# Kernel tuning notes

Measured on AMD Instinct MI355X. Metric: run time of the kernel, lower is better.

The kernel has to match this reference:

```python
import jax, jax.numpy as jnp
import numpy as np
from jax import lax

NPOINT = 1024
K = 32
GN_GROUPS = 32
EPS = 1e-5


def farthest_point_sample(xyz, npoint):
    # xyz: (B,N,3) -> idx (B,npoint). Deterministic start at index 0.
    B, N, _ = xyz.shape
    dist0 = jnp.full((B, N), 1e10, dtype=xyz.dtype)
    far0 = jnp.zeros((B,), dtype=jnp.int32)
    barange = jnp.arange(B)

    def step(carry, _):
        dist, far = carry
        centroid = xyz[barange, far][:, None, :]              # (B,1,3)
        d = jnp.sum((xyz - centroid) ** 2, axis=-1)           # (B,N)
        dist = jnp.minimum(dist, d)
        far_new = jnp.argmax(dist, axis=-1).astype(jnp.int32)
        return (dist, far_new), far

    _, idxs = lax.scan(step, (dist0, far0), None, length=npoint)
    return idxs.T  # (B,npoint)


def conv1x1(x, w, b):
    # x: (B,Cin,M,K), w: (Cout,Cin)
    return jnp.einsum('oc,bcmk->bomk', w, x) + b[None, :, None, None]


def group_norm(x, gamma, beta, groups):
    B, C, M, Kk = x.shape
    xg = x.reshape(B, groups, C // groups, M, Kk)
    mu = xg.mean(axis=(2, 3, 4), keepdims=True)
    var = xg.var(axis=(2, 3, 4), keepdims=True)
    xg = (xg - mu) * lax.rsqrt(var + EPS)
    x = xg.reshape(B, C, M, Kk)
    return x * gamma[None, :, None, None] + beta[None, :, None, None]


def setup_inputs() -> dict:
    key = jax.random.key(0)
    ks = jax.random.split(key, 4)
    B, N, Cin = 16, 8192, 64
    hid, out_ch, in_total = 64, 128, 3 + Cin
    return {
        'xyz': jax.random.normal(ks[0], (B, N, 3), jnp.float32),
        'feat': jax.random.normal(ks[1], (B, N, Cin), jnp.float32),
        'w1': jax.random.normal(ks[2], (hid, in_total), jnp.float32) * 0.1,
        'b1': jnp.zeros((hid,), jnp.float32),
        'g1w': jnp.ones((hid,), jnp.float32),
        'g1b': jnp.zeros((hid,), jnp.float32),
        'w2': jax.random.normal(ks[3], (out_ch, hid), jnp.float32) * 0.1,
        'b2': jnp.zeros((out_ch,), jnp.float32),
        'g2w': jnp.ones((out_ch,), jnp.float32),
        'g2b': jnp.zeros((out_ch,), jnp.float32),
    }


def reference(xyz, feat, w1, b1, g1w, g1b, w2, b2, g2w, g2b):
    B, N, _ = xyz.shape
    M = min(NPOINT, N)
    k = min(K, N)

    fps_idx = farthest_point_sample(lax.stop_gradient(xyz), M)   # (B,M) ints
    batch = jnp.arange(B)[:, None]
    centroids = xyz[batch, fps_idx]                              # (B,M,3)

    # kNN via squared distances (same ordering as cdist p=2)
    d2 = (jnp.sum(centroids ** 2, -1)[:, :, None]
          + jnp.sum(xyz ** 2, -1)[:, None, :]
          - 2.0 * jnp.einsum('bmd,bnd->bmn', centroids, xyz))    # (B,M,N)
    knn_idx = lax.top_k(-d2, k)[1]                               # (B,M,k)

    b3 = jnp.arange(B)[:, None, None]
    group_xyz = xyz[b3, knn_idx]                                 # (B,M,k,3)
    delta = group_xyz - centroids[:, :, None, :]
    gfeat = feat[b3, knn_idx]                                    # (B,M,k,Cin)
    gf = jnp.concatenate([delta, gfeat], axis=-1)                # (B,M,k,3+Cin)
    x = jnp.transpose(gf, (0, 3, 1, 2))                          # (B,C,M,k)

    x = jax.nn.relu(group_norm(conv1x1(x, w1, b1), g1w, g1b, GN_GROUPS))
    x = jax.nn.relu(group_norm(conv1x1(x, w2, b2), g2w, g2b, GN_GROUPS))
    out = jnp.max(x, axis=-1)                                    # (B,out_ch,M)
    new_feat = jnp.transpose(out, (0, 2, 1))                     # (B,M,out_ch)
    return (centroids, new_feat)
```

## Files before the change

kernel.cpp:

```cpp
#include <hip/hip_runtime.h>
#include <cstdint>

#define BB 16
#define NN 8192
#define MM 1024
#define KNN 32
#define CIN 64
#define HID 64
#define OCH 128

#define KNN_OFF   0u
#define SUM1_OFF  524288u
#define SUM2_OFF  526336u
#define A1_OFF    530432u
#define D1_OFF    531456u
#define A2_OFF    532480u
#define D2_OFF    534528u
#define W2B_OFF   536576u
#define W1B_OFF   540672u
#define Y1_OFF    543744u
#define PTS4_OFF  Y1_OFF
#define FEAT16_OFF (Y1_OFF + 16777216u)

typedef unsigned long long u64;
typedef float f32x4 __attribute__((ext_vector_type(4)));
typedef float f32x2 __attribute__((ext_vector_type(2)));
typedef short bf16x8 __attribute__((ext_vector_type(8)));

__device__ __forceinline__ unsigned short f2bf(float f) {
  union { float f; unsigned u; } v; v.f = f;
  unsigned r = v.u + 0x7FFFu + ((v.u >> 16) & 1u);
  return (unsigned short)(r >> 16);
}

__device__ __forceinline__ float bf2f(unsigned short u) {
  return __uint_as_float((unsigned)u << 16);
}

__global__ __launch_bounds__(256) void k0_init(const float* __restrict__ xyz,
                                               const float* __restrict__ feat,
                                               const float* __restrict__ w1,
                                               const float* __restrict__ w2,
                                               float* __restrict__ ws) {
  int t = blockIdx.x * 256 + threadIdx.x;
  if (t < 12288) ws[SUM1_OFF + t] = 0.0f;
  if (t < 4096) {
    unsigned lo = f2bf(w2[2 * t]);
    unsigned hi = f2bf(w2[2 * t + 1]);
    ((unsigned*)(ws + W2B_OFF))[t] = lo | (hi << 16);
  }
  if (t < 6144) {
    int n = t / 96, kk = t % 96;
    float val = 0.0f;
    if (kk < 3) val = w1[n * 67 + kk];
    else if (kk >= 4 && kk < 68) val = w1[n * 67 + kk - 1];
    ((unsigned short*)(ws + W1B_OFF))[t] = f2bf(val);
  }
  if (t < BB * NN) {
    #pragma clang fp contract(off)
    float x = xyz[(size_t)t * 3], y = xyz[(size_t)t * 3 + 1], z = xyz[(size_t)t * 3 + 2];
    ((float4*)(ws + PTS4_OFF))[t] = make_float4(x, y, z, (x * x + y * y) + z * z);
  }
  if (t < 4194304) {
    float2 fv = *(const float2*)(feat + 2 * (size_t)t);
    unsigned lo = f2bf(fv.x), hi = f2bf(fv.y);
    ((unsigned*)(ws + FEAT16_OFF))[t] = lo | (hi << 16);
  }
}

__device__ __forceinline__ u64 wave_max_u64(u64 v) {
  #define DPP_RND(ctrl, rm)                                                     \
  {                                                                             \
    int lo_ = __builtin_amdgcn_update_dpp(0, (int)(unsigned)(v & 0xFFFFFFFFull),\
                                          ctrl, rm, 0xf, true);                 \
    int hi_ = __builtin_amdgcn_update_dpp(0, (int)(unsigned)(v >> 32),          \
                                          ctrl, rm, 0xf, true);                 \
    u64 o_ = ((u64)(unsigned)hi_ << 32) | (unsigned)lo_;                        \
    v = o_ > v ? o_ : v;                                                        \
  }
  DPP_RND(0x111, 0xf)
  DPP_RND(0x112, 0xf)
  DPP_RND(0x114, 0xf)
  DPP_RND(0x118, 0xf)
  DPP_RND(0x142, 0xa)
  DPP_RND(0x143, 0xc)
  #undef DPP_RND
  return v;
}

__global__ __launch_bounds__(256) void fps_kernel(const float* __restrict__ xyz,
                                                  float* __restrict__ cent) {
  #pragma clang fp contract(off)
  __shared__ float4 sp4[NN];
  __shared__ u64 slots[MM];
  __shared__ u64 wred[2][4];
  const int b = blockIdx.x, tid = threadIdx.x;
  const int w = tid >> 6;
  const float* xp = xyz + (size_t)b * NN * 3;
  f32x2 px[16], py[16], pz[16];
  float dist0[16], dist1[16];
  #pragma unroll
  for (int i = 0; i < 16; ++i) {
    int n0 = tid + (2 * i) * 256, n1 = tid + (2 * i + 1) * 256;
    float x0 = xp[n0 * 3], y0 = xp[n0 * 3 + 1], z0 = xp[n0 * 3 + 2];
    float x1 = xp[n1 * 3], y1 = xp[n1 * 3 + 1], z1 = xp[n1 * 3 + 2];
    px[i] = (f32x2){x0, x1}; py[i] = (f32x2){y0, y1}; pz[i] = (f32x2){z0, z1};
    sp4[n0] = make_float4(x0, y0, z0, 0.0f);
    sp4[n1] = make_float4(x1, y1, z1, 0.0f);
    dist0[i] = 1e10f; dist1[i] = 1e10f;
  }
  __syncthreads();
  int far = 0;
  for (int step = 0; step < MM; ++step) {
    float4 c4 = sp4[far];
    f32x2 cx = (f32x2){c4.x, c4.x}, cy = (f32x2){c4.y, c4.y}, cz = (f32x2){c4.z, c4.z};
    float best = -1.0f;
    #pragma unroll
    for (int i = 0; i < 16; ++i) {
      f32x2 dx = px[i] - cx, dy = py[i] - cy, dz = pz[i] - cz;
      f32x2 d = (dx * dx + dy * dy) + dz * dz;
      float dm0 = fminf(dist0[i], d.x);
      float dm1 = fminf(dist1[i], d.y);
      dist0[i] = dm0; dist1[i] = dm1;
      best = fmaxf(fmaxf(best, dm0), dm1);
    }
    unsigned sel[16];
    #pragma unroll
    for (int i = 0; i < 16; ++i) {
      unsigned s0 = (dist0[i] == best) ? (unsigned)(2 * i) : 63u;
      unsigned s1 = (dist1[i] == best) ? (unsigned)(2 * i + 1) : 63u;
      sel[i] = s0 < s1 ? s0 : s1;
    }
    #pragma unroll
    for (int st = 8; st >= 1; st >>= 1)
      #pragma unroll
      for (int i = 0; i < st; ++i)
        sel[i] = sel[i] < sel[i + st] ? sel[i] : sel[i + st];
    int bi = tid + (int)(sel[0] << 8);
    u64 key = ((u64)__float_as_uint(best) << 32) | (unsigned)(8191 - bi);
    key = wave_max_u64(key);
    const int p = step & 1;
    if ((tid & 63) == 63) wred[p][w] = key;
    __syncthreads();
    u64 k0 = wred[p][0], k1 = wred[p][1], k2 = wred[p][2], k3 = wred[p][3];
    u64 m01 = k0 > k1 ? k0 : k1;
    u64 m23 = k2 > k3 ? k2 : k3;
    u64 bk = m01 > m23 ? m01 : m23;
    if (tid == 0) slots[step] = bk;
    far = 8191 - (int)(unsigned)(bk & 0xFFFFFFFFull);
  }
  __syncthreads();
  float* co = cent + (size_t)b * MM * 3;
  for (int s = tid; s < MM; s += 256) {
    int fs = (s == 0) ? 0 : (8191 - (int)(unsigned)(slots[s - 1] & 0xFFFFFFFFull));
    float4 c = sp4[fs];
    co[s * 3 + 0] = c.x; co[s * 3 + 1] = c.y; co[s * 3 + 2] = c.z;
  }
}

__global__ __launch_bounds__(512) void knn_kernel(const float4* __restrict__ pts4,
                                                  const float* __restrict__ cent,
                                                  int* __restrict__ knnout) {
  #pragma clang fp contract(off)
  __shared__ __align__(16) char smem[65536];
  unsigned* blo = (unsigned*)smem;
  unsigned* bhi = (unsigned*)(smem + 32768);
  u64* marea = (u64*)smem;
  const int tid = threadIdx.x;
  const int lane = tid & 63;
  const int w = tid >> 6;
  const int b = blockIdx.x >> 4;
  const int m = ((blockIdx.x & 15) << 6) + lane;
  const float* cp = cent + ((size_t)b * MM + m) * 3;
  float cx = cp[0], cy = cp[1], cz = cp[2];
  float cn2 = (cx * cx + cy * cy) + cz * cz;
  u64 key[32];
  {
    u64 initk = ((u64)(__float_as_uint(3e38f) ^ 0x80000000u) << 32) | 0xFFFFFFFFull;
    #pragma unroll
    for (int j = 0; j < 32; ++j) key[j] = initk;
  }
  float kthf = 3e38f;

  auto insert = [&](u64 cand) {
    bool cprev = false; u64 kprev = 0;
    #pragma unroll
    for (int j = 0; j < 32; ++j) {
      bool cj = cand < key[j];
      u64 cur = key[j];
      u64 nv = cj ? cand : cur;
      key[j] = cprev ? kprev : nv;
      cprev = cj; kprev = cur;
    }
    unsigned hb = (unsigned)(key[31] >> 32);
    unsigned ob = (hb & 0x80000000u) ? (hb ^ 0x80000000u) : ~hb;
    kthf = __uint_as_float(ob);
  };

  int cnt = 0;
  auto flush = [&]() {
    int mc = cnt;
    #pragma unroll
    for (int off = 1; off < 64; off <<= 1) { int o = __shfl_xor(mc, off); mc = o > mc ? o : mc; }
    for (int i = 0; i < mc; ++i) {
      u64 cand = ((u64)bhi[i * 512 + tid] << 32) | blo[i * 512 + tid];
      if (i < cnt && cand < key[31]) insert(cand);
    }
    cnt = 0;
  };

  const int nbase = __builtin_amdgcn_readfirstlane(w * 1024);
  const float4* pb = pts4 + (size_t)b * NN + nbase;
  for (int n0 = 0; n0 < 1024; n0 += 8) {
    #pragma unroll
    for (int j = 0; j < 8; ++j) {
      int n = n0 + j;
      float4 p = pb[n];
      float dot = fmaf(cz, p.z, fmaf(cy, p.y, cx * p.x));
      float d2 = (cn2 + p.w) - 2.0f * dot;
      if (d2 <= kthf) {
        unsigned db = __float_as_uint(d2);
        unsigned fk = db ^ (((int)db < 0) ? 0xFFFFFFFFu : 0x80000000u);
        blo[cnt * 512 + tid] = (unsigned)(nbase + n);
        bhi[cnt * 512 + tid] = fk;
        cnt++;
      }
    }
    if (__ballot(cnt >= 9)) flush();
  }
  flush();
  __syncthreads();

  auto publish = [&](int a) {
    u64* ap = marea + a * 2048;
    #pragma unroll
    for (int j = 0; j < 32; ++j) ap[j * 64 + lane] = key[j];
  };
  auto merge_from = [&](int a) {
    u64* ap = marea + a * 2048;
    for (int j = 0; j < 32; ++j) {
      u64 cand = ap[j * 64 + lane];
      if (cand < key[31]) insert(cand);
    }
  };
  if (w & 1) publish(w >> 1);
  __syncthreads();
  if (!(w & 1)) merge_from(w >> 1);
  __syncthreads();
  if (w == 2) publish(0);
  if (w == 6) publish(1);
  __syncthreads();
  if (w == 0) merge_from(0);
  if (w == 4) merge_from(1);
  __syncthreads();
  if (w == 4) publish(0);
  __syncthreads();
  if (w == 0) {
    merge_from(0);
    int* op = knnout + ((size_t)b * MM + m) * KNN;
    #pragma unroll
    for (int j = 0; j < 32; ++j) op[j] = (int)(key[j] & 0xFFFFFFFFull);
  }
}

__global__ __launch_bounds__(256) void conv1_kernel(const float* __restrict__ xyz,
                                                    const unsigned short* __restrict__ feat16,
                                                    const float* __restrict__ cent,
                                                    const int* __restrict__ knn,
                                                    const unsigned short* __restrict__ w1b,
                                                    const float* __restrict__ b1,
                                                    float* __restrict__ y1,
                                                    float* __restrict__ sums1) {
  __shared__ __align__(16) unsigned short gsm[4][32 * 104];
  __shared__ float s1acc[64], q1acc[64];
  const int tid = threadIdx.x, lane = tid & 63, w = tid >> 6;
  const int wid = blockIdx.x * 4 + w;
  const int b = wid >> 10;
  unsigned short* gf = gsm[w];

  if (tid < 64) { s1acc[tid] = 0.0f; q1acc[tid] = 0.0f; }
  __syncthreads();

  int idxv = 0;
  if (lane < 32) idxv = knn[(size_t)wid * 32 + lane];

  {
    int row = lane >> 1, h = (lane & 1) * 16;
    ushort4 z4 = {0, 0, 0, 0};
    *(ushort4*)(gf + row * 104 + 64 + h + 0)  = z4;
    *(ushort4*)(gf + row * 104 + 64 + h + 4)  = z4;
    *(ushort4*)(gf + row * 104 + 64 + h + 8)  = z4;
    *(ushort4*)(gf + row * 104 + 64 + h + 12) = z4;
  }
  const float* cp = cent + (size_t)wid * 3;
  float ccx = cp[0], ccy = cp[1], ccz = cp[2];
  if (lane < 32) {
    const float* pp = xyz + ((size_t)b * NN + idxv) * 3;
    ushort4 dv;
    dv.x = f2bf(pp[0] - ccx); dv.y = f2bf(pp[1] - ccy); dv.z = f2bf(pp[2] - ccz);
    dv.w = 0;
    *(ushort4*)(gf + lane * 104) = dv;
  }
  const unsigned short* fb = feat16 + (size_t)b * NN * 64;
  #pragma unroll
  for (int i = 0; i < 4; ++i) {
    int v = i * 64 + lane;
    int row = v >> 3, part = v & 7;
    int ridx = __shfl(idxv, row);
    uint4 fv = *(const uint4*)(fb + (size_t)ridx * 64 + part * 8);
    *(uint2*)(gf + row * 104 + 4 + part * 8)     = make_uint2(fv.x, fv.y);
    *(uint2*)(gf + row * 104 + 4 + part * 8 + 4) = make_uint2(fv.z, fv.w);
  }
  __builtin_amdgcn_s_waitcnt(0);
  __builtin_amdgcn_wave_barrier();

  const int quad = lane >> 4, lr = lane & 15;
  bf16x8 bw[4][3];
  float b1v[4];
  #pragma unroll
  for (int nt = 0; nt < 4; ++nt) {
    #pragma unroll
    for (int ks = 0; ks < 3; ++ks)
      bw[nt][ks] = *(const bf16x8*)(w1b + (size_t)(nt * 16 + lr) * 96 + ks * 32 + quad * 8);
    b1v[nt] = b1[nt * 16 + lr];
  }
  f32x4 acc[2][4];
  #pragma unroll
  for (int mt = 0; mt < 2; ++mt)
    #pragma unroll
    for (int nt = 0; nt < 4; ++nt)
      acc[mt][nt] = (f32x4){0.f, 0.f, 0.f, 0.f};
  #pragma unroll
  for (int ks = 0; ks < 3; ++ks) {
    bf16x8 a0 = *(const bf16x8*)(gf + (0 + lr) * 104 + ks * 32 + quad * 8);
    bf16x8 a1 = *(const bf16x8*)(gf + (16 + lr) * 104 + ks * 32 + quad * 8);
    #pragma unroll
    for (int nt = 0; nt < 4; ++nt) {
      acc[0][nt] = __builtin_amdgcn_mfma_f32_16x16x32_bf16(a0, bw[nt][ks], acc[0][nt], 0, 0, 0);
      acc[1][nt] = __builtin_amdgcn_mfma_f32_16x16x32_bf16(a1, bw[nt][ks], acc[1][nt], 0, 0, 0);
    }
  }
  unsigned short* yo16 = (unsigned short*)(y1 + (size_t)wid * 1024);
  float s_nt[4] = {0.f, 0.f, 0.f, 0.f};
  float q_nt[4] = {0.f, 0.f, 0.f, 0.f};
  #pragma unroll
  for (int mt = 0; mt < 2; ++mt)
    #pragma unroll
    for (int rg = 0; rg < 4; ++rg) {
      int row = mt * 16 + quad * 4 + rg;
      #pragma unroll
      for (int nt = 0; nt < 4; ++nt) {
        float z = acc[mt][nt][rg] + b1v[nt];
        yo16[row * 64 + nt * 16 + lr] = f2bf(z);
        s_nt[nt] += z;
        q_nt[nt] = fmaf(z, z, q_nt[nt]);
      }
    }
  #pragma unroll
  for (int nt = 0; nt < 4; ++nt) {
    float s = s_nt[nt], q = q_nt[nt];
    s += __shfl_xor(s, 16); s += __shfl_xor(s, 32);
    q += __shfl_xor(q, 16); q += __shfl_xor(q, 32);
    if (quad == 0) {
      atomicAdd(&s1acc[nt * 16 + lr], s);
      atomicAdd(&q1acc[nt * 16 + lr], q);
    }
  }
  __syncthreads();
  if (tid < 64) {
    atomicAdd(&sums1[b * 128 + tid], s1acc[tid]);
    atomicAdd(&sums1[b * 128 + 64 + tid], q1acc[tid]);
  }
}

struct Conv2Frag {
  bf16x8 bfr[8][2];
  float  b2v[8];
};

__device__ __forceinline__ void load_w2_frags(const unsigned short* __restrict__ w2b,
                                              const float* __restrict__ b2,
                                              int lane, Conv2Frag& F) {
  const int quad = lane >> 4, lr = lane & 15;
  #pragma unroll
  for (int nt = 0; nt < 8; ++nt) {
    #pragma unroll
    for (int t = 0; t < 2; ++t)
      F.bfr[nt][t] = *(const bf16x8*)(w2b + (size_t)(nt * 16 + lr) * 64 + t * 32 + quad * 8);
    F.b2v[nt] = b2[nt * 16 + lr];
  }
}

__device__ __forceinline__ void conv2_wave_mfma(const float* __restrict__ y1,
                                                const float* a1s,
                                                const float* d1s,
                                                unsigned short* __restrict__ hrow,
                                                int wid, int lane,
                                                const Conv2Frag& F,
                                                f32x4 acc[2][8]) {
  const int quad = lane >> 4, lr = lane & 15;
  const int r = lane >> 1, c0 = (lane & 1) * 32;
  const unsigned short* yrow16 =
      (const unsigned short*)(y1 + (size_t)wid * 1024) + r * 64 + c0;
  const float4* ap = (const float4*)(a1s + c0);
  const float4* dp = (const float4*)(d1s + c0);
  #pragma unroll
  for (int gg = 0; gg < 4; ++gg) {
    bf16x8 yv = *(const bf16x8*)(yrow16 + gg * 8);
    float4 av0 = ap[gg * 2],     dv0 = dp[gg * 2];
    float4 av1 = ap[gg * 2 + 1], dv1 = dp[gg * 2 + 1];
    ushort4 s0, s1;
    s0.x = f2bf(fmaxf(0.0f, fmaf(bf2f((unsigned short)yv[0]), av0.x, dv0.x)));
    s0.y = f2bf(fmaxf(0.0f, fmaf(bf2f((unsigned short)yv[1]), av0.y, dv0.y)));
    s0.z = f2bf(fmaxf(0.0f, fmaf(bf2f((unsigned short)yv[2]), av0.z, dv0.z)));
    s0.w = f2bf(fmaxf(0.0f, fmaf(bf2f((unsigned short)yv[3]), av0.w, dv0.w)));
    s1.x = f2bf(fmaxf(0.0f, fmaf(bf2f((unsigned short)yv[4]), av1.x, dv1.x)));
    s1.y = f2bf(fmaxf(0.0f, fmaf(bf2f((unsigned short)yv[5]), av1.y, dv1.y)));
    s1.z = f2bf(fmaxf(0.0f, fmaf(bf2f((unsigned short)yv[6]), av1.z, dv1.z)));
    s1.w = f2bf(fmaxf(0.0f, fmaf(bf2f((unsigned short)yv[7]), av1.w, dv1.w)));
    *(ushort4*)(hrow + r * 72 + c0 + 8 * gg)     = s0;
    *(ushort4*)(hrow + r * 72 + c0 + 8 * gg + 4) = s1;
  }
  __builtin_amdgcn_s_waitcnt(0);
  __builtin_amdgcn_wave_barrier();
  #pragma unroll
  for (int mt = 0; mt < 2; ++mt)
    #pragma unroll
    for (int nt = 0; nt < 8; ++nt)
      acc[mt][nt] = (f32x4){0.f, 0.f, 0.f, 0.f};
  #pragma unroll
  for (int t = 0; t < 2; ++t) {
    bf16x8 a0 = *(const bf16x8*)(hrow + (0 + lr) * 72 + t * 32 + quad * 8);
    bf16x8 a1f = *(const bf16x8*)(hrow + (16 + lr) * 72 + t * 32 + quad * 8);
    #pragma unroll
    for (int nt = 0; nt < 8; ++nt) {
      acc[0][nt] = __builtin_amdgcn_mfma_f32_16x16x32_bf16(a0,  F.bfr[nt][t], acc[0][nt], 0, 0, 0);
      acc[1][nt] = __builtin_amdgcn_mfma_f32_16x16x32_bf16(a1f, F.bfr[nt][t], acc[1][nt], 0, 0, 0);
    }
  }
}

__global__ __launch_bounds__(256) void conv2_stats_kernel(float* __restrict__ y1,
                                                          const float* __restrict__ sums1,
                                                          const float* __restrict__ g1w,
                                                          const float* __restrict__ g1b,
                                                          const unsigned short* __restrict__ w2b,
                                                          const float* __restrict__ b2,
                                                          float* __restrict__ sums2) {
  __shared__ __align__(16) unsigned short hsm[4][32 * 72];
  __shared__ float sacc[128], qacc[128];
  __shared__ float a1s[64], d1s[64];
  const int tid = threadIdx.x, lane = tid & 63, w = tid >> 6;
  const int wid = blockIdx.x * 4 + w;
  const int b = blockIdx.x >> 8;
  if (tid < 128) { sacc[tid] = 0.0f; qacc[tid] = 0.0f; }
  if (tid < 64) {
    int c = tid, g = c >> 1;
    float S = sums1[b * 128 + g * 2] + sums1[b * 128 + g * 2 + 1];
    float Q = sums1[b * 128 + 64 + g * 2] + sums1[b * 128 + 64 + g * 2 + 1];
    float mu = S * (1.0f / 65536.0f);
    float var = Q * (1.0f / 65536.0f) - mu * mu;
    float rs = 1.0f / sqrtf(var + 1e-5f);
    float ga = g1w[c];
    a1s[c] = rs * ga;
    d1s[c] = g1b[c] - mu * rs * ga;
  }
  __syncthreads();
  Conv2Frag F;
  load_w2_frags(w2b, b2, lane, F);
  f32x4 acc[2][8];
  conv2_wave_mfma(y1, a1s, d1s, hsm[w], wid, lane, F, acc);
  const int lr = lane & 15;
  float zmx[8], zmn[8];
  #pragma unroll
  for (int nt = 0; nt < 8; ++nt) {
    float s = 0, q = 0, mx = -3e38f, mn = 3e38f;
    #pragma unroll
    for (int mt = 0; mt < 2; ++mt)
      #pragma unroll
      for (int rg = 0; rg < 4; ++rg) {
        float z = acc[mt][nt][rg] + F.b2v[nt];
        s += z; q = fmaf(z, z, q);
        mx = fmaxf(mx, z); mn = fminf(mn, z);
      }
    atomicAdd(&sacc[nt * 16 + lr], s);
    atomicAdd(&qacc[nt * 16 + lr], q);
    mx = fmaxf(mx, __shfl_xor(mx, 16)); mx = fmaxf(mx, __shfl_xor(mx, 32));
    mn = fminf(mn, __shfl_xor(mn, 16)); mn = fminf(mn, __shfl_xor(mn, 32));
    zmx[nt] = mx; zmn[nt] = mn;
  }
  if (lane < 16) {
    float* zp = y1 + (size_t)wid * 1024;
    #pragma unroll
    for (int nt = 0; nt < 8; ++nt) {
      zp[nt * 16 + lr] = zmx[nt];
      zp[128 + nt * 16 + lr] = zmn[nt];
    }
  }
  __syncthreads();
  if (tid < 128) {
    atomicAdd(&sums2[b * 256 + tid], sacc[tid]);
    atomicAdd(&sums2[b * 256 + 128 + tid], qacc[tid]);
  }
}

__global__ __launch_bounds__(256) void final_lite(const float* __restrict__ y1,
                                                  const float* __restrict__ sums2,
                                                  const float* __restrict__ g2w,
                                                  const float* __restrict__ g2b,
                                                  float* __restrict__ nf) {
  __shared__ float a2s[128], d2s[128];
  const int tid = threadIdx.x;
  const int wid0 = blockIdx.x * 2;
  const int b = wid0 >> 10;
  if (tid < 128) {
    int c = tid, g = c >> 2;
    float S = ((sums2[b * 256 + g * 4] + sums2[b * 256 + g * 4 + 1])
               + sums2[b * 256 + g * 4 + 2]) + sums2[b * 256 + g * 4 + 3];
    float Q = ((sums2[b * 256 + 128 + g * 4] + sums2[b * 256 + 128 + g * 4 + 1])
               + sums2[b * 256 + 128 + g * 4 + 2]) + sums2[b * 256 + 128 + g * 4 + 3];
    float mu = S * (1.0f / 131072.0f);
    float var = Q * (1.0f / 131072.0f) - mu * mu;
    float rs = 1.0f / sqrtf(var + 1e-5f);
    float ga = g2w[c];
    a2s[c] = rs * ga;
    d2s[c] = g2b[c] - mu * rs * ga;
  }
  __syncthreads();
  int wid = wid0 + (tid >> 7), c = tid & 127;
  const float* zp = y1 + (size_t)wid * 1024;
  float zmx = zp[c];
  float zmn = zp[128 + c];
  float az = a2s[c], dz = d2s[c];
  float z = (az >= 0.0f) ? zmx : zmn;
  nf[(size_t)wid * 128 + c] = fmaxf(0.0f, fmaf(z, az, dz));
}

extern "C" void kernel_launch(void* const* d_in, const int* in_sizes, int n_in,
                              void* d_out, int out_size, void* d_ws, size_t ws_size,
                              hipStream_t stream) {
  const float* xyz  = (const float*)d_in[0];
  const float* feat = (const float*)d_in[1];
  const float* w1   = (const float*)d_in[2];
  const float* b1   = (const float*)d_in[3];
  const float* g1w  = (const float*)d_in[4];
  const float* g1b  = (const float*)d_in[5];
  const float* w2   = (const float*)d_in[6];
  const float* b2   = (const float*)d_in[7];
  const float* g2w  = (const float*)d_in[8];
  const float* g2b  = (const float*)d_in[9];
  float* ws = (float*)d_ws;
  float* cent = (float*)d_out;
  float* nf   = (float*)d_out + BB * MM * 3;
  const float4* pts4 = (const float4*)(ws + PTS4_OFF);
  int*   knn   = (int*)(ws + KNN_OFF);
  float* sums1 = ws + SUM1_OFF;
  float* sums2 = ws + SUM2_OFF;
  const unsigned short* w2b = (const unsigned short*)(ws + W2B_OFF);
  const unsigned short* w1b = (const unsigned short*)(ws + W1B_OFF);
  const unsigned short* feat16 = (const unsigned short*)(ws + FEAT16_OFF);
  float* y1 = ws + Y1_OFF;

  hipLaunchKernelGGL(k0_init, dim3(16384), dim3(256), 0, stream, xyz, feat, w1, w2, ws);
  hipLaunchKernelGGL(fps_kernel, dim3(16), dim3(256), 0, stream, xyz, cent);
  hipLaunchKernelGGL(knn_kernel, dim3(256), dim3(512), 0, stream, pts4, cent, knn);
  hipLaunchKernelGGL(conv1_kernel, dim3(4096), dim3(256), 0, stream,
                     xyz, feat16, cent, knn, w1b, b1, y1, sums1);
  hipLaunchKernelGGL(conv2_stats_kernel, dim3(4096), dim3(256), 0, stream,
                     y1, sums1, g1w, g1b, w2b, b2, sums2);
  hipLaunchKernelGGL(final_lite, dim3(8192), dim3(256), 0, stream,
                     y1, sums2, g2w, g2b, nf);
}
```

Before: 1.592 ms.

## Fuse init work into FPS kernel and simplify per-step argmax reduction

```diff
diff --git a/kernel.cpp b/kernel.cpp
--- a/kernel.cpp
+++ b/kernel.cpp
@@ -12,10 +12,6 @@
 #define KNN_OFF   0u
 #define SUM1_OFF  524288u
 #define SUM2_OFF  526336u
-#define A1_OFF    530432u
-#define D1_OFF    531456u
-#define A2_OFF    532480u
-#define D2_OFF    534528u
 #define W2B_OFF   536576u
 #define W1B_OFF   540672u
 #define Y1_OFF    543744u
@@ -35,37 +31,6 @@
 
 __device__ __forceinline__ float bf2f(unsigned short u) {
   return __uint_as_float((unsigned)u << 16);
-}
-
-__global__ __launch_bounds__(256) void k0_init(const float* __restrict__ xyz,
-                                               const float* __restrict__ feat,
-                                               const float* __restrict__ w1,
-                                               const float* __restrict__ w2,
-                                               float* __restrict__ ws) {
-  int t = blockIdx.x * 256 + threadIdx.x;
-  if (t < 12288) ws[SUM1_OFF + t] = 0.0f;
-  if (t < 4096) {
-    unsigned lo = f2bf(w2[2 * t]);
-    unsigned hi = f2bf(w2[2 * t + 1]);
-    ((unsigned*)(ws + W2B_OFF))[t] = lo | (hi << 16);
-  }
-  if (t < 6144) {
-    int n = t / 96, kk = t % 96;
-    float val = 0.0f;
-    if (kk < 3) val = w1[n * 67 + kk];
-    else if (kk >= 4 && kk < 68) val = w1[n * 67 + kk - 1];
-    ((unsigned short*)(ws + W1B_OFF))[t] = f2bf(val);
-  }
-  if (t < BB * NN) {
-    #pragma clang fp contract(off)
-    float x = xyz[(size_t)t * 3], y = xyz[(size_t)t * 3 + 1], z = xyz[(size_t)t * 3 + 2];
-    ((float4*)(ws + PTS4_OFF))[t] = make_float4(x, y, z, (x * x + y * y) + z * z);
-  }
-  if (t < 4194304) {
-    float2 fv = *(const float2*)(feat + 2 * (size_t)t);
-    unsigned lo = f2bf(fv.x), hi = f2bf(fv.y);
-    ((unsigned*)(ws + FEAT16_OFF))[t] = lo | (hi << 16);
-  }
 }
 
 __device__ __forceinline__ u64 wave_max_u64(u64 v) {
@@ -88,14 +53,46 @@
   return v;
 }
 
-__global__ __launch_bounds__(256) void fps_kernel(const float* __restrict__ xyz,
-                                                  float* __restrict__ cent) {
+__global__ __launch_bounds__(256) void fps_init_kernel(const float* __restrict__ xyz,
+                                                       const float* __restrict__ feat,
+                                                       const float* __restrict__ w1,
+                                                       const float* __restrict__ w2,
+                                                       float* __restrict__ ws,
+                                                       float* __restrict__ cent) {
   #pragma clang fp contract(off)
   __shared__ float4 sp4[NN];
   __shared__ u64 slots[MM];
-  __shared__ u64 wred[2][4];
-  const int b = blockIdx.x, tid = threadIdx.x;
-  const int w = tid >> 6;
+  const int tid = threadIdx.x;
+
+  if (blockIdx.x >= 16) {
+    const int t0 = (blockIdx.x - 16) * 256 + tid;
+    const int stride = 240 * 256;
+    for (int t = t0; t < 12288; t += stride) ws[SUM1_OFF + t] = 0.0f;
+    for (int t = t0; t < 4096; t += stride) {
+      unsigned lo = f2bf(w2[2 * t]);
+      unsigned hi = f2bf(w2[2 * t + 1]);
+      ((unsigned*)(ws + W2B_OFF))[t] = lo | (hi << 16);
+    }
+    for (int t = t0; t < 6144; t += stride) {
+      int n = t / 96, kk = t % 96;
+      float val = 0.0f;
+      if (kk < 3) val = w1[n * 67 + kk];
+      else if (kk >= 4 && kk < 68) val = w1[n * 67 + kk - 1];
+      ((unsigned short*)(ws + W1B_OFF))[t] = f2bf(val);
+    }
+    for (int t = t0; t < BB * NN; t += stride) {
+      float x = xyz[(size_t)t * 3], y = xyz[(size_t)t * 3 + 1], z = xyz[(size_t)t * 3 + 2];
+      ((float4*)(ws + PTS4_OFF))[t] = make_float4(x, y, z, (x * x + y * y) + z * z);
+    }
+    for (int t = t0; t < 4194304; t += stride) {
+      float2 fv = *(const float2*)(feat + 2 * (size_t)t);
+      unsigned lo = f2bf(fv.x), hi = f2bf(fv.y);
+      ((unsigned*)(ws + FEAT16_OFF))[t] = lo | (hi << 16);
+    }
+    return;
+  }
+
+  const int b = blockIdx.x;
   const float* xp = xyz + (size_t)b * NN * 3;
   f32x2 px[16], py[16], pz[16];
   float dist0[16], dist1[16];
@@ -109,12 +106,13 @@
     sp4[n1] = make_float4(x1, y1, z1, 0.0f);
     dist0[i] = 1e10f; dist1[i] = 1e10f;
   }
+  for (int s = tid; s < MM; s += 256) slots[s] = 0ull;
   __syncthreads();
   int far = 0;
   for (int step = 0; step < MM; ++step) {
     float4 c4 = sp4[far];
     f32x2 cx = (f32x2){c4.x, c4.x}, cy = (f32x2){c4.y, c4.y}, cz = (f32x2){c4.z, c4.z};
-    float best = -1.0f;
+    float best = -1.0f; int bi = 0;
     #pragma unroll
     for (int i = 0; i < 16; ++i) {
       f32x2 dx = px[i] - cx, dy = py[i] - cy, dz = pz[i] - cz;
@@ -122,34 +120,15 @@
       float dm0 = fminf(dist0[i], d.x);
       float dm1 = fminf(dist1[i], d.y);
       dist0[i] = dm0; dist1[i] = dm1;
-      best = fmaxf(fmaxf(best, dm0), dm1);
-    }
-    unsigned sel[16];
-    #pragma unroll
-    for (int i = 0; i < 16; ++i) {
-      unsigned s0 = (dist0[i] == best) ? (unsigned)(2 * i) : 63u;
-      unsigned s1 = (dist1[i] == best) ? (unsigned)(2 * i + 1) : 63u;
-      sel[i] = s0 < s1 ? s0 : s1;
-    }
-    #pragma unroll
-    for (int st = 8; st >= 1; st >>= 1)
-      #pragma unroll
-      for (int i = 0; i < st; ++i)
-        sel[i] = sel[i] < sel[i + st] ? sel[i] : sel[i + st];
-    int bi = tid + (int)(sel[0] << 8);
+      if (dm0 > best) { best = dm0; bi = tid + (2 * i) * 256; }
+      if (dm1 > best) { best = dm1; bi = tid + (2 * i + 1) * 256; }
+    }
     u64 key = ((u64)__float_as_uint(best) << 32) | (unsigned)(8191 - bi);
     key = wave_max_u64(key);
-    const int p = step & 1;
-    if ((tid & 63) == 63) wred[p][w] = key;
+    if ((tid & 63) == 63) atomicMax(&slots[step], key);
     __syncthreads();
-    u64 k0 = wred[p][0], k1 = wred[p][1], k2 = wred[p][2], k3 = wred[p][3];
-    u64 m01 = k0 > k1 ? k0 : k1;
-    u64 m23 = k2 > k3 ? k2 : k3;
-    u64 bk = m01 > m23 ? m01 : m23;
-    if (tid == 0) slots[step] = bk;
-    far = 8191 - (int)(unsigned)(bk & 0xFFFFFFFFull);
-  }
-  __syncthreads();
+    far = 8191 - (int)(unsigned)(slots[step] & 0xFFFFFFFFull);
+  }
   float* co = cent + (size_t)b * MM * 3;
   for (int s = tid; s < MM; s += 256) {
     int fs = (s == 0) ? 0 : (8191 - (int)(unsigned)(slots[s - 1] & 0xFFFFFFFFull));
@@ -561,8 +540,8 @@
   const unsigned short* feat16 = (const unsigned short*)(ws + FEAT16_OFF);
   float* y1 = ws + Y1_OFF;
 
-  hipLaunchKernelGGL(k0_init, dim3(16384), dim3(256), 0, stream, xyz, feat, w1, w2, ws);
-  hipLaunchKernelGGL(fps_kernel, dim3(16), dim3(256), 0, stream, xyz, cent);
+  hipLaunchKernelGGL(fps_init_kernel, dim3(256), dim3(256), 0, stream,
+                     xyz, feat, w1, w2, ws, cent);
   hipLaunchKernelGGL(knn_kernel, dim3(256), dim3(512), 0, stream, pts4, cent, knn);
   hipLaunchKernelGGL(conv1_kernel, dim3(4096), dim3(256), 0, stream,
                      xyz, feat16, cent, knn, w1b, b1, y1, sums1);
```

Result: faster. 1.447 ms (-9.1%).
